# Kernel tuning notes

Measured on AMD Instinct MI355X. Metric: run time of the kernel, lower is better.

## Reference

```python
import jax, jax.numpy as jnp
import numpy as np

N, E, G = 50000, 800000, 128      # nodes, edges, graphs
IN, H, OUT = 128, 128, 2          # feature dims
K, L = 3, 3                       # Chebyshev order, num conv layers
EPS = 1e-5


def setup_inputs() -> dict:
    key = jax.random.key(0)
    ks = jax.random.split(key, 10)
    x = jax.random.normal(ks[0], (N, IN), dtype=jnp.float32)
    edge_index = jax.random.randint(ks[1], (2, E), 0, N, dtype=jnp.int64)
    batch = jnp.sort(jax.random.randint(ks[2], (N,), 0, G, dtype=jnp.int64))
    w_in = jax.random.normal(ks[3], (IN, H), dtype=jnp.float32) * 0.05
    b_in = jnp.zeros((H,), jnp.float32)
    ln_g = jnp.ones((H,), jnp.float32)
    ln_b = jnp.zeros((H,), jnp.float32)
    cheb_w = jax.random.normal(ks[4], (L, K, H, H), dtype=jnp.float32) * 0.05
    cheb_b = jnp.zeros((L, H), jnp.float32)
    bn_g = jnp.ones((L, H), jnp.float32)
    bn_b = jnp.zeros((L, H), jnp.float32)
    w1 = jax.random.normal(ks[5], (H, H // 2), dtype=jnp.float32) * 0.05
    b1 = jnp.zeros((H // 2,), jnp.float32)
    w2 = jax.random.normal(ks[6], (H // 2, OUT), dtype=jnp.float32) * 0.05
    b2 = jnp.zeros((OUT,), jnp.float32)
    return dict(x=x, w_in=w_in, b_in=b_in, ln_g=ln_g, ln_b=ln_b,
                cheb_w=cheb_w, cheb_b=cheb_b, bn_g=bn_g, bn_b=bn_b,
                w1=w1, b1=b1, w2=w2, b2=b2,
                edge_index=edge_index, batch=batch)


def reference(x, w_in, b_in, ln_g, ln_b, cheb_w, cheb_b, bn_g, bn_b,
              w1, b1, w2, b2, edge_index, batch):
    src, dst = edge_index[0], edge_index[1]

    # ChebConv scaled Laplacian with lambda_max=2, sym norm:
    # L_hat = -D^{-1/2} A D^{-1/2}  (self-loop terms cancel in PyG's __norm__)
    deg = jax.ops.segment_sum(jnp.ones((E,), x.dtype), src, num_segments=N)
    dinv = jnp.where(deg > 0, jax.lax.rsqrt(jnp.maximum(deg, 1.0)), 0.0)
    w_edge = -dinv[src] * dinv[dst]  # [E]

    def spmm(h):  # y_i = sum_{(j->i)} w_edge * h_j
        return jax.ops.segment_sum(w_edge[:, None] * h[src], dst, num_segments=N)

    # node_embed: Linear -> LayerNorm -> ReLU (dropout p used in eval => identity)
    h = x @ w_in + b_in
    mu = h.mean(-1, keepdims=True)
    var = h.var(-1, keepdims=True)
    h = (h - mu) * jax.lax.rsqrt(var + EPS) * ln_g + ln_b
    h = jax.nn.relu(h)

    hiddens = [h]
    for l in range(L):
        # Chebyshev recurrence: T0 = h, T1 = L_hat h, Tk = 2 L_hat T_{k-1} - T_{k-2}
        tx0 = h
        out = tx0 @ cheb_w[l, 0]
        tx1 = spmm(tx0)
        out = out + tx1 @ cheb_w[l, 1]
        for k in range(2, K):
            tx2 = 2.0 * spmm(tx1) - tx0
            out = out + tx2 @ cheb_w[l, k]
            tx0, tx1 = tx1, tx2
        out = out + cheb_b[l]
        # BatchNorm1d over nodes (training-mode batch statistics, biased var)
        m = out.mean(0)
        v = out.var(0)
        out = (out - m) * jax.lax.rsqrt(v + EPS) * bn_g[l] + bn_b[l]
        h = jax.nn.relu(out)
        hiddens.append(h)

    # Laplacian (Dirichlet) regularization over all hidden states
    reg = jnp.float32(0.0)
    for hh in hiddens:
        diff = hh[src] - hh[dst]              # [E, H]
        reg = reg + jnp.mean(jnp.sum(diff * diff, axis=-1))
    reg = reg / len(hiddens)

    # global mean pool over batch assignment
    counts = jax.ops.segment_sum(jnp.ones((N,), x.dtype), batch, num_segments=G)
    gsum = jax.ops.segment_sum(h, batch, num_segments=G)
    gmean = gsum / jnp.maximum(counts, 1.0)[:, None]

    z = jax.nn.relu(gmean @ w1 + b1)
    logits = z @ w2 + b2
    return logits, reg
```

## Files before the change

### kernel.cpp

```cpp
#include <hip/hip_runtime.h>
#include <hip/hip_bf16.h>

#define NNODES 50000
#define NEDGES 800000
#define NGRAPH 128
#define CAP 64
#define EPSV 1e-5f

typedef __attribute__((ext_vector_type(8))) short bf16x8;
typedef __attribute__((ext_vector_type(8))) unsigned short us16x8;
typedef __attribute__((ext_vector_type(4))) float f32x4;
typedef __attribute__((ext_vector_type(2))) float f32x2;

__device__ __forceinline__ unsigned short f2bf(float f) {
    unsigned u = __float_as_uint(f);
    return (unsigned short)((u + 0x7fffu + ((u >> 16) & 1u)) >> 16);
}
__device__ __forceinline__ float bf2f(unsigned short h) {
    return __uint_as_float(((unsigned)h) << 16);
}
__device__ __forceinline__ unsigned pk4_fp8(float a, float b, float c, float d) {
    int w = __builtin_amdgcn_cvt_pk_fp8_f32(a, b, 0, false);
    w = __builtin_amdgcn_cvt_pk_fp8_f32(c, d, w, true);
    return (unsigned)w;
}

__global__ void fillA_kernel(const int* __restrict__ src, const int* __restrict__ dst,
                             int* __restrict__ outdeg, int* __restrict__ indeg,
                             unsigned* __restrict__ slot, int E) {
    int e = blockIdx.x * blockDim.x + threadIdx.x;
    if (e < E) {
        int s = src[e];
        int d = dst[e];
        atomicAdd(&outdeg[s], 1);
        int pos = atomicAdd(&indeg[d], 1);
        if (pos < CAP) slot[(size_t)d * CAP + pos] = (unsigned)s;
    }
}

__global__ void dinv_gstart_kernel(const int* __restrict__ outdeg, float* __restrict__ dinv,
                                   const int* __restrict__ batch, int* __restrict__ gstart, int n) {
    int i = blockIdx.x * blockDim.x + threadIdx.x;
    if (i < n) {
        int d = outdeg[i];
        dinv[i] = (d > 0) ? rsqrtf((float)d) : 0.0f;
    }
    if (blockIdx.x == 0 && threadIdx.x <= NGRAPH) {
        int g = threadIdx.x;
        int lo = 0, hi = n;
        while (lo < hi) {
            int mid = (lo + hi) >> 1;
            if (batch[mid] < g) lo = mid + 1; else hi = mid;
        }
        gstart[g] = lo;
    }
}

__global__ void pack_kernel(unsigned* __restrict__ slot, const int* __restrict__ indeg,
                            const float* __restrict__ dinv, int total) {
    int i = blockIdx.x * blockDim.x + threadIdx.x;
    if (i >= total) return;
    int node = i >> 6, k = i & (CAP - 1);
    int cnt = min(indeg[node], CAP);
    if (k < cnt) {
        unsigned idx = slot[i];
        slot[i] = idx | ((unsigned)f2bf(dinv[idx]) << 16);
    }
}

__global__ void wprep_kernel(const float* __restrict__ w_in, const float* __restrict__ cheb_w,
                             unsigned short* __restrict__ Wsp) {
    int p = blockIdx.x;
    int t = threadIdx.x;
    for (int s8 = 0; s8 < 8; ++s8) {
        int slot = s8 * 256 + t;
        int kc = slot >> 9, ct = (slot >> 6) & 7, lane = slot & 63;
        int q = lane >> 4, nn = lane & 15;
        unsigned short* o = Wsp + ((size_t)p * 2048 + slot) * 16;
#pragma unroll
        for (int j = 0; j < 8; ++j) {
            int k = kc * 32 + q * 8 + j, c = ct * 16 + nn;
            float v;
            if (p == 0) {
                v = w_in[k * 128 + c];
            } else {
                int pl = (p - 1) / 3, kk = (p - 1) % 3;
                v = cheb_w[((size_t)(pl * 3 + kk) * 128 + k) * 128 + c];
                if (kk == 0) v -= cheb_w[((size_t)(pl * 3 + 2) * 128 + k) * 128 + c];
                else if (kk == 2) v *= 2.f;
            }
            unsigned short hi = f2bf(v);
            o[j] = hi;
            o[8 + j] = f2bf(v - bf2f(hi));
        }
    }
}

template <int NPARTS, int EPI, int AF32>
__global__ __launch_bounds__(256) void gemm_mfma(
    const void* __restrict__ A0v, const void* __restrict__ A1v, const void* __restrict__ A2v,
    const unsigned short* __restrict__ Wsp, const float* __restrict__ bias,
    unsigned short* __restrict__ out16,
    const float* __restrict__ g0, const float* __restrict__ b0,
    float* __restrict__ colsum, float* __restrict__ colsumsq, int n) {
    __shared__ float red[256];
    int t = threadIdx.x, w = t >> 6, l = t & 63;
    int m = l & 15, qk = l >> 4;
    int rowA = blockIdx.x * 64 + w * 16 + m;
    red[t] = 0.f;
    __syncthreads();

    f32x4 acc[8];
#pragma unroll
    for (int ct = 0; ct < 8; ++ct) acc[ct] = (f32x4){0.f, 0.f, 0.f, 0.f};

    bool valid = rowA < n;
#pragma unroll
    for (int p = 0; p < NPARTS; ++p) {
#pragma unroll
        for (int kc = 0; kc < 4; ++kc) {
            bf16x8 ah, al;
            if (AF32) {
                const float* arow = (const float*)A0v;
                if (p == 1) arow = (const float*)A1v;
                if (p == 2) arow = (const float*)A2v;
                arow += (size_t)rowA * 128;
                float4 x0, x1;
                if (valid) {
                    x0 = *(const float4*)&arow[kc * 32 + qk * 8];
                    x1 = *(const float4*)&arow[kc * 32 + qk * 8 + 4];
                } else {
                    x0 = make_float4(0.f, 0.f, 0.f, 0.f); x1 = x0;
                }
                float xs[8] = {x0.x, x0.y, x0.z, x0.w, x1.x, x1.y, x1.z, x1.w};
#pragma unroll
                for (int j = 0; j < 8; ++j) {
                    unsigned short hi = f2bf(xs[j]);
                    ah[j] = (short)hi;
                    al[j] = (short)f2bf(xs[j] - bf2f(hi));
                }
            } else {
                const unsigned short* arow = (const unsigned short*)A0v;
                if (p == 1) arow = (const unsigned short*)A1v;
                if (p == 2) arow = (const unsigned short*)A2v;
                arow += (size_t)rowA * 128;
                if (valid) ah = *(const bf16x8*)&arow[kc * 32 + qk * 8];
                else ah = (bf16x8){0, 0, 0, 0, 0, 0, 0, 0};
            }
            const unsigned short* wb = Wsp + ((size_t)((p * 4 + kc) * 8) * 64 + l) * 16;
#pragma unroll
            for (int ct = 0; ct < 8; ++ct) {
                bf16x8 bh = *(const bf16x8*)(wb + (size_t)ct * 64 * 16);
                bf16x8 bl = *(const bf16x8*)(wb + (size_t)ct * 64 * 16 + 8);
                acc[ct] = __builtin_amdgcn_mfma_f32_16x16x32_bf16(ah, bh, acc[ct], 0, 0, 0);
                if (AF32)
                    acc[ct] = __builtin_amdgcn_mfma_f32_16x16x32_bf16(al, bh, acc[ct], 0, 0, 0);
                acc[ct] = __builtin_amdgcn_mfma_f32_16x16x32_bf16(ah, bl, acc[ct], 0, 0, 0);
            }
        }
    }

    int rowC0 = blockIdx.x * 64 + w * 16 + qk * 4;
    if (EPI == 0) {
        float rs[4] = {0.f, 0.f, 0.f, 0.f}, rss[4] = {0.f, 0.f, 0.f, 0.f};
#pragma unroll
        for (int ct = 0; ct < 8; ++ct) {
            float b = bias[ct * 16 + m];
#pragma unroll
            for (int j = 0; j < 4; ++j) {
                float v = acc[ct][j] + b;
                acc[ct][j] = v;
                rs[j] += v; rss[j] += v * v;
            }
        }
#pragma unroll
        for (int off = 1; off < 16; off <<= 1) {
#pragma unroll
            for (int j = 0; j < 4; ++j) {
                rs[j] += __shfl_xor(rs[j], off, 64);
                rss[j] += __shfl_xor(rss[j], off, 64);
            }
        }
        float mean[4], rstd[4];
#pragma unroll
        for (int j = 0; j < 4; ++j) {
            mean[j] = rs[j] * (1.f / 128.f);
            float var = rss[j] * (1.f / 128.f) - mean[j] * mean[j];
            rstd[j] = rsqrtf(var + EPSV);
        }
#pragma unroll
        for (int ct = 0; ct < 8; ++ct) {
            int c = ct * 16 + m;
            float gg = g0[c], bb = b0[c];
#pragma unroll
            for (int j = 0; j < 4; ++j) {
                int gr = rowC0 + j;
                if (gr < n) {
                    float x = (acc[ct][j] - mean[j]) * rstd[j] * gg + bb;
                    x = fmaxf(x, 0.f);
                    out16[(size_t)gr * 128 + c] = f2bf(x);
                }
            }
        }
    } else {
#pragma unroll
        for (int ct = 0; ct < 8; ++ct) {
            int c = ct * 16 + m;
            float b = bias[c];
            float s = 0.f, ss = 0.f;
#pragma unroll
            for (int j = 0; j < 4; ++j) {
                int gr = rowC0 + j;
                if (gr < n) {
                    float v = acc[ct][j] + b;
                    out16[(size_t)gr * 128 + c] = f2bf(v);
                    s += v; ss += v * v;
                }
            }
            s += __shfl_xor(s, 16, 64);  ss += __shfl_xor(ss, 16, 64);
            s += __shfl_xor(s, 32, 64);  ss += __shfl_xor(ss, 32, 64);
            if (qk == 0) {
                atomicAdd(&red[c], s);
                atomicAdd(&red[128 + c], ss);
            }
        }
        __syncthreads();
        if (t < 128) {
            atomicAdd(&colsum[t], red[t]);
            atomicAdd(&colsumsq[t], red[128 + t]);
        }
    }
}

__global__ void repack8_kernel(const unsigned short* __restrict__ h16,
                               unsigned char* __restrict__ h8, int total8) {
    int i = blockIdx.x * blockDim.x + threadIdx.x;
    if (i >= total8) return;
    us16x8 a = ((const us16x8*)h16)[i];
    uint2 o;
    o.x = pk4_fp8(bf2f(a[0]), bf2f(a[1]), bf2f(a[2]), bf2f(a[3]));
    o.y = pk4_fp8(bf2f(a[4]), bf2f(a[5]), bf2f(a[6]), bf2f(a[7]));
    ((uint2*)h8)[i] = o;
}

template <int MODE>
__global__ void spmm_g(const unsigned char* __restrict__ g8,
                       const unsigned short* __restrict__ self16,
                       unsigned short* __restrict__ dst16, unsigned char* __restrict__ dst8,
                       const unsigned* __restrict__ slot,
                       const float* __restrict__ dinv,
                       const int* __restrict__ outdeg, const int* __restrict__ indeg,
                       int n, double* __restrict__ norm_slots, double* __restrict__ cross_slots) {
    int w = (int)((blockIdx.x * (unsigned)blockDim.x + threadIdx.x) >> 6);
    if (w >= n) return;
    int lane = threadIdx.x & 63;
    int g = lane >> 4;
    int q = lane & 15;
    int cnt = min(indeg[w], CAP);
    float hi[8];
    if (MODE != 1) {
        us16x8 a = *(const us16x8*)&self16[(size_t)w * 128 + q * 8];
#pragma unroll
        for (int j = 0; j < 8; ++j) hi[j] = bf2f(a[j]);
    }
    float acc[8];
#pragma unroll
    for (int j = 0; j < 8; ++j) acc[j] = 0.f;
    float cr = 0.f;
    unsigned cw = 0;
    if (lane < cnt) cw = slot[(size_t)w * CAP + lane];
    int idx = (int)(cw & 0xFFFFu);
    float dv = bf2f((unsigned short)(cw >> 16));
    int iters = (cnt + 31) >> 5;
    for (int it = 0; it < iters; ++it) {
        int sb = (it << 5) + (g << 3);
        int jj[8]; float dd[8];
#pragma unroll
        for (int u = 0; u < 8; ++u) {
            jj[u] = __shfl(idx, sb + u, 64);
            dd[u] = __shfl(dv, sb + u, 64);
        }
        uint2 uu[8];
#pragma unroll
        for (int u = 0; u < 8; ++u) {
            uu[u] = make_uint2(0, 0);
            if (sb + u < cnt) uu[u] = *(const uint2*)&g8[(size_t)jj[u] * 128 + q * 8];
        }
#pragma unroll
        for (int u = 0; u < 8; ++u) {
            f32x2 l0 = __builtin_amdgcn_cvt_pk_f32_fp8(uu[u].x, false);
            f32x2 h0 = __builtin_amdgcn_cvt_pk_f32_fp8(uu[u].x, true);
            f32x2 l1 = __builtin_amdgcn_cvt_pk_f32_fp8(uu[u].y, false);
            f32x2 h1 = __builtin_amdgcn_cvt_pk_f32_fp8(uu[u].y, true);
            float v[8] = {l0.x, l0.y, h0.x, h0.y, l1.x, l1.y, h1.x, h1.y};
            if (MODE != 2) {
#pragma unroll
                for (int j = 0; j < 8; ++j) acc[j] += dd[u] * v[j];
            }
            if (MODE != 1) {
#pragma unroll
                for (int j = 0; j < 8; ++j) cr += hi[j] * v[j];
            }
        }
    }
    if (MODE != 2) {
#pragma unroll
        for (int j = 0; j < 8; ++j) {
            acc[j] += __shfl_xor(acc[j], 16, 64);
            acc[j] += __shfl_xor(acc[j], 32, 64);
        }
        if (g == 0) {
            float di = dinv[w];
            float v[8];
            us16x8 o;
#pragma unroll
            for (int j = 0; j < 8; ++j) { v[j] = -di * acc[j]; o[j] = f2bf(v[j]); }
            *(us16x8*)&dst16[(size_t)w * 128 + q * 8] = o;
            if (MODE == 0) {
                uint2 o8;
                o8.x = pk4_fp8(v[0], v[1], v[2], v[3]);
                o8.y = pk4_fp8(v[4], v[5], v[6], v[7]);
                *(uint2*)&dst8[(size_t)w * 128 + q * 8] = o8;
            }
        }
    }
    if (MODE != 1) {
        float nt = 0.f;
#pragma unroll
        for (int j = 0; j < 8; ++j) nt += hi[j] * hi[j];
        nt *= 0.25f;
        for (int off = 32; off > 0; off >>= 1) {
            cr += __shfl_down(cr, off, 64);
            nt += __shfl_down(nt, off, 64);
        }
        if (lane == 0) {
            int slotid = w & 255;
            atomicAdd(&cross_slots[slotid], (double)cr);
            atomicAdd(&norm_slots[slotid], (double)nt * (double)(outdeg[w] + indeg[w]));
        }
    }
}

__global__ void bnrelu_kernel(const unsigned short* __restrict__ ob16,
                              const float* __restrict__ colsum, const float* __restrict__ colsumsq,
                              const float* __restrict__ bn_g, const float* __restrict__ bn_b,
                              unsigned short* __restrict__ h16, unsigned char* __restrict__ h8,
                              int n, int total4) {
    __shared__ float ssc[128], ssh[128];
    int t = threadIdx.x;
    if (t < 128) {
        float m = colsum[t] / (float)n;
        float v = colsumsq[t] / (float)n - m * m;
        float sc = bn_g[t] * rsqrtf(v + EPSV);
        ssc[t] = sc;
        ssh[t] = bn_b[t] - m * sc;
    }
    __syncthreads();
    int i = blockIdx.x * blockDim.x + t;
    if (i >= total4) return;
    ushort4 o = ((const ushort4*)ob16)[i];
    int c = (i * 4) & 127;
    float4 r;
    r.x = fmaxf(bf2f(o.x) * ssc[c + 0] + ssh[c + 0], 0.f);
    r.y = fmaxf(bf2f(o.y) * ssc[c + 1] + ssh[c + 1], 0.f);
    r.z = fmaxf(bf2f(o.z) * ssc[c + 2] + ssh[c + 2], 0.f);
    r.w = fmaxf(bf2f(o.w) * ssc[c + 3] + ssh[c + 3], 0.f);
    ushort4 u = make_ushort4(f2bf(r.x), f2bf(r.y), f2bf(r.z), f2bf(r.w));
    ((ushort4*)h16)[i] = u;
    ((unsigned*)h8)[i] = pk4_fp8(r.x, r.y, r.z, r.w);
}

__global__ void poolmlp_kernel(const unsigned short* __restrict__ h16, const int* __restrict__ start,
                               const float* __restrict__ w1, const float* __restrict__ b1,
                               const float* __restrict__ w2, const float* __restrict__ b2,
                               const double* __restrict__ norm_slots,
                               const double* __restrict__ cross_slots,
                               float* __restrict__ out) {
    __shared__ float sm[2][128];
    __shared__ float gm[128];
    int g = blockIdx.x, t = threadIdx.x;
    int half = t >> 7, c = t & 127;
    int s = start[g], e = start[g + 1];
    float acc = 0.f;
    for (int r = s + half; r < e; r += 2) acc += bf2f(h16[(size_t)r * 128 + c]);
    sm[half][c] = acc;
    __syncthreads();
    if (t < 128) {
        float cnt = fmaxf((float)(e - s), 1.f);
        gm[t] = (sm[0][t] + sm[1][t]) / cnt;
    }
    __syncthreads();
    if (t < 64) {
        float z = b1[t];
        for (int k = 0; k < 128; ++k) z += gm[k] * w1[(size_t)k * 64 + t];
        z = fmaxf(z, 0.f);
        float p0 = z * w2[t * 2 + 0];
        float p1 = z * w2[t * 2 + 1];
        for (int off = 32; off > 0; off >>= 1) {
            p0 += __shfl_down(p0, off, 64);
            p1 += __shfl_down(p1, off, 64);
        }
        if (t == 0) {
            out[g * 2 + 0] = p0 + b2[0];
            out[g * 2 + 1] = p1 + b2[1];
        }
    } else if (g == 0 && t < 128) {
        int l = t - 64;
        double ns = 0.0, cs = 0.0;
        for (int i = l; i < 256; i += 64) { ns += norm_slots[i]; cs += cross_slots[i]; }
        for (int off = 32; off > 0; off >>= 1) {
            ns += __shfl_down(ns, off, 64);
            cs += __shfl_down(cs, off, 64);
        }
        if (l == 0) out[256] = (float)((ns - 2.0 * cs) / ((double)NEDGES * 4.0));
    }
}

extern "C" void kernel_launch(void* const* d_in, const int* in_sizes, int n_in,
                              void* d_out, int out_size, void* d_ws, size_t ws_size,
                              hipStream_t stream) {
    const float* x      = (const float*)d_in[0];
    const float* w_in   = (const float*)d_in[1];
    const float* b_in   = (const float*)d_in[2];
    const float* ln_g   = (const float*)d_in[3];
    const float* ln_b   = (const float*)d_in[4];
    const float* cheb_w = (const float*)d_in[5];
    const float* cheb_b = (const float*)d_in[6];
    const float* bn_g   = (const float*)d_in[7];
    const float* bn_b   = (const float*)d_in[8];
    const float* w1     = (const float*)d_in[9];
    const float* b1     = (const float*)d_in[10];
    const float* w2     = (const float*)d_in[11];
    const float* b2     = (const float*)d_in[12];
    const int*   eidx   = (const int*)d_in[13];
    const int*   batch  = (const int*)d_in[14];
    const int* src = eidx;
    const int* dst = eidx + NEDGES;
    float* out = (float*)d_out;

    char* ws = (char*)d_ws;
    size_t off = 0;
    auto alloc = [&](size_t bytes) -> void* {
        void* p = ws + off;
        off = (off + bytes + 255) & ~(size_t)255;
        return p;
    };
    unsigned short* ob16 = (unsigned short*)alloc((size_t)NNODES * 128 * 2);
    unsigned short* h16  = (unsigned short*)alloc((size_t)NNODES * 128 * 2);
    unsigned short* t116 = (unsigned short*)alloc((size_t)NNODES * 128 * 2);
    unsigned short* s16  = (unsigned short*)alloc((size_t)NNODES * 128 * 2);
    unsigned char*  h8   = (unsigned char*)alloc((size_t)NNODES * 128);
    unsigned char*  t18  = (unsigned char*)alloc((size_t)NNODES * 128);
    unsigned short* Wsp  = (unsigned short*)alloc((size_t)10 * 2048 * 16 * 2);
    int* degs     = (int*)alloc((size_t)2 * NNODES * 4);
    int* outdeg   = degs;
    int* indeg    = degs + NNODES;
    float* dinv   = (float*)alloc((size_t)NNODES * 4);
    unsigned* slot = (unsigned*)alloc((size_t)NNODES * CAP * 4);
    int* gstart   = (int*)alloc((size_t)(NGRAPH + 1) * 4);
    float* colstats = (float*)alloc(768 * 4 + 512 * 8);
    double* dslots  = (double*)(colstats + 768);
    double* norm_slots  = dslots;
    double* cross_slots = dslots + 256;

    hipMemsetAsync(degs, 0, (size_t)2 * NNODES * 4, stream);
    hipMemsetAsync(colstats, 0, 768 * 4 + 512 * 8, stream);

    int tE = (NEDGES + 255) / 256;
    int tN = (NNODES + 255) / 256;
    fillA_kernel<<<tE, 256, 0, stream>>>(src, dst, outdeg, indeg, slot, NEDGES);
    dinv_gstart_kernel<<<tN, 256, 0, stream>>>(outdeg, dinv, batch, gstart, NNODES);
    pack_kernel<<<(NNODES * CAP + 255) / 256, 256, 0, stream>>>(slot, indeg, dinv, NNODES * CAP);
    wprep_kernel<<<10, 256, 0, stream>>>(w_in, cheb_w, Wsp);

    int gemmBlocks = (NNODES + 63) / 64;
    int waveBlocks = (NNODES * 64 + 255) / 256;
    int total4 = NNODES * 128 / 4;
    int total8 = NNODES * 128 / 8;

    gemm_mfma<1, 0, 1><<<gemmBlocks, 256, 0, stream>>>(x, nullptr, nullptr, Wsp, b_in, h16,
                                                       ln_g, ln_b, nullptr, nullptr, NNODES);
    repack8_kernel<<<(total8 + 255) / 256, 256, 0, stream>>>(h16, h8, total8);

    for (int l = 0; l < 3; ++l) {
        float* colsum = colstats + 256 * l;
        float* colsumsq = colsum + 128;
        spmm_g<0><<<waveBlocks, 256, 0, stream>>>(h8, h16, t116, t18, slot, dinv,
                                                  outdeg, indeg, NNODES, norm_slots, cross_slots);
        spmm_g<1><<<waveBlocks, 256, 0, stream>>>(t18, nullptr, s16, nullptr, slot, dinv,
                                                  outdeg, indeg, NNODES, nullptr, nullptr);
        gemm_mfma<3, 1, 0><<<gemmBlocks, 256, 0, stream>>>(h16, t116, s16,
            Wsp + (size_t)(1 + 3 * l) * 2048 * 16, cheb_b + (size_t)l * 128, ob16,
            nullptr, nullptr, colsum, colsumsq, NNODES);
        bnrelu_kernel<<<(total4 + 255) / 256, 256, 0, stream>>>(ob16, colsum, colsumsq,
            bn_g + (size_t)l * 128, bn_b + (size_t)l * 128, h16, h8, NNODES, total4);
    }
    spmm_g<2><<<waveBlocks, 256, 0, stream>>>(h8, h16, nullptr, nullptr, slot, dinv,
                                              outdeg, indeg, NNODES, norm_slots, cross_slots);

    poolmlp_kernel<<<NGRAPH, 256, 0, stream>>>(h16, gstart, w1, b1, w2, b2,
                                               norm_slots, cross_slots, out);
}
```

Before: 738.5 us.

## Map four nodes per wavefront in SpMM with 16-lane groups per node

The SpMM/Dirichlet kernel now gives each node a 16-lane group, so one wavefront handles four nodes instead of one. Each group loads its own edge slots in chunks of 16 and gathers neighbour rows itself. This removes the cross-group xor-shuffle reduction, the duplicated self-row reads and the 0.25 norm correction. It targets the lanes that sat idle when a node's in-degree (about 16 on average) was far below the 32-edge iteration width. The cost is more divergence between groups with different degrees, and each group now walks its edges serially in chunks of 16.

```diff
diff --git a/kernel.cpp b/kernel.cpp
--- a/kernel.cpp
+++ b/kernel.cpp
@@ -251,43 +251,45 @@
                        const float* __restrict__ dinv,
                        const int* __restrict__ outdeg, const int* __restrict__ indeg,
                        int n, double* __restrict__ norm_slots, double* __restrict__ cross_slots) {
-    int w = (int)((blockIdx.x * (unsigned)blockDim.x + threadIdx.x) >> 6);
-    if (w >= n) return;
     int lane = threadIdx.x & 63;
     int g = lane >> 4;
     int q = lane & 15;
-    int cnt = min(indeg[w], CAP);
+    int w = (int)((blockIdx.x * (unsigned)blockDim.x + threadIdx.x) >> 6) * 4 + g;
+    bool active = w < n;
+    int cnt = active ? min(indeg[w], CAP) : 0;
+    size_t rbase = (size_t)w * 128 + q * 8;
     float hi[8];
     if (MODE != 1) {
-        us16x8 a = *(const us16x8*)&self16[(size_t)w * 128 + q * 8];
-#pragma unroll
-        for (int j = 0; j < 8; ++j) hi[j] = bf2f(a[j]);
+#pragma unroll
+        for (int j = 0; j < 8; ++j) hi[j] = 0.f;
+        if (active) {
+            us16x8 a = *(const us16x8*)&self16[rbase];
+#pragma unroll
+            for (int j = 0; j < 8; ++j) hi[j] = bf2f(a[j]);
+        }
     }
     float acc[8];
 #pragma unroll
     for (int j = 0; j < 8; ++j) acc[j] = 0.f;
     float cr = 0.f;
-    unsigned cw = 0;
-    if (lane < cnt) cw = slot[(size_t)w * CAP + lane];
-    int idx = (int)(cw & 0xFFFFu);
-    float dv = bf2f((unsigned short)(cw >> 16));
-    int iters = (cnt + 31) >> 5;
-    for (int it = 0; it < iters; ++it) {
-        int sb = (it << 5) + (g << 3);
-        int jj[8]; float dd[8];
-#pragma unroll
-        for (int u = 0; u < 8; ++u) {
-            jj[u] = __shfl(idx, sb + u, 64);
-            dd[u] = __shfl(dv, sb + u, 64);
-        }
-        uint2 uu[8];
-#pragma unroll
-        for (int u = 0; u < 8; ++u) {
+    size_t sbase = (size_t)w * CAP;
+#pragma unroll
+    for (int c = 0; c < 4; ++c) {
+        if (c * 16 >= cnt) break;
+        unsigned cw = (c * 16 + q < cnt) ? slot[sbase + c * 16 + q] : 0u;
+        int mycnt = min(cnt - c * 16, 16);
+        uint2 uu[16];
+        float dd[16];
+#pragma unroll
+        for (int u = 0; u < 16; ++u) {
+            unsigned cwu = __shfl(cw, (g << 4) + u, 64);
+            int j = (int)(cwu & 0xFFFFu);
+            dd[u] = bf2f((unsigned short)(cwu >> 16));
             uu[u] = make_uint2(0, 0);
-            if (sb + u < cnt) uu[u] = *(const uint2*)&g8[(size_t)jj[u] * 128 + q * 8];
-        }
-#pragma unroll
-        for (int u = 0; u < 8; ++u) {
+            if (u < mycnt) uu[u] = *(const uint2*)&g8[(size_t)j * 128 + q * 8];
+        }
+#pragma unroll
+        for (int u = 0; u < 16; ++u) {
             f32x2 l0 = __builtin_amdgcn_cvt_pk_f32_fp8(uu[u].x, false);
             f32x2 h0 = __builtin_amdgcn_cvt_pk_f32_fp8(uu[u].x, true);
             f32x2 l1 = __builtin_amdgcn_cvt_pk_f32_fp8(uu[u].y, false);
@@ -303,37 +305,30 @@
             }
         }
     }
-    if (MODE != 2) {
-#pragma unroll
-        for (int j = 0; j < 8; ++j) {
-            acc[j] += __shfl_xor(acc[j], 16, 64);
-            acc[j] += __shfl_xor(acc[j], 32, 64);
-        }
-        if (g == 0) {
-            float di = dinv[w];
-            float v[8];
-            us16x8 o;
-#pragma unroll
-            for (int j = 0; j < 8; ++j) { v[j] = -di * acc[j]; o[j] = f2bf(v[j]); }
-            *(us16x8*)&dst16[(size_t)w * 128 + q * 8] = o;
-            if (MODE == 0) {
-                uint2 o8;
-                o8.x = pk4_fp8(v[0], v[1], v[2], v[3]);
-                o8.y = pk4_fp8(v[4], v[5], v[6], v[7]);
-                *(uint2*)&dst8[(size_t)w * 128 + q * 8] = o8;
-            }
+    if (MODE != 2 && active) {
+        float di = dinv[w];
+        float v[8];
+        us16x8 o;
+#pragma unroll
+        for (int j = 0; j < 8; ++j) { v[j] = -di * acc[j]; o[j] = f2bf(v[j]); }
+        *(us16x8*)&dst16[rbase] = o;
+        if (MODE == 0) {
+            uint2 o8;
+            o8.x = pk4_fp8(v[0], v[1], v[2], v[3]);
+            o8.y = pk4_fp8(v[4], v[5], v[6], v[7]);
+            *(uint2*)&dst8[(size_t)w * 128 + q * 8] = o8;
         }
     }
     if (MODE != 1) {
         float nt = 0.f;
 #pragma unroll
         for (int j = 0; j < 8; ++j) nt += hi[j] * hi[j];
-        nt *= 0.25f;
-        for (int off = 32; off > 0; off >>= 1) {
-            cr += __shfl_down(cr, off, 64);
-            nt += __shfl_down(nt, off, 64);
-        }
-        if (lane == 0) {
+#pragma unroll
+        for (int off = 8; off > 0; off >>= 1) {
+            cr += __shfl_down(cr, off, 16);
+            nt += __shfl_down(nt, off, 16);
+        }
+        if (q == 0 && active) {
             int slotid = w & 255;
             atomicAdd(&cross_slots[slotid], (double)cr);
             atomicAdd(&norm_slots[slotid], (double)nt * (double)(outdeg[w] + indeg[w]));
@@ -474,7 +469,8 @@
     wprep_kernel<<<10, 256, 0, stream>>>(w_in, cheb_w, Wsp);
 
     int gemmBlocks = (NNODES + 63) / 64;
-    int waveBlocks = (NNODES * 64 + 255) / 256;
+    int nodes4 = (NNODES + 3) / 4;
+    int spmmBlocks = (nodes4 * 64 + 255) / 256;
     int total4 = NNODES * 128 / 4;
     int total8 = NNODES * 128 / 8;
 
@@ -485,9 +481,9 @@
     for (int l = 0; l < 3; ++l) {
         float* colsum = colstats + 256 * l;
         float* colsumsq = colsum + 128;
-        spmm_g<0><<<waveBlocks, 256, 0, stream>>>(h8, h16, t116, t18, slot, dinv,
+        spmm_g<0><<<spmmBlocks, 256, 0, stream>>>(h8, h16, t116, t18, slot, dinv,
                                                   outdeg, indeg, NNODES, norm_slots, cross_slots);
-        spmm_g<1><<<waveBlocks, 256, 0, stream>>>(t18, nullptr, s16, nullptr, slot, dinv,
+        spmm_g<1><<<spmmBlocks, 256, 0, stream>>>(t18, nullptr, s16, nullptr, slot, dinv,
                                                   outdeg, indeg, NNODES, nullptr, nullptr);
         gemm_mfma<3, 1, 0><<<gemmBlocks, 256, 0, stream>>>(h16, t116, s16,
             Wsp + (size_t)(1 + 3 * l) * 2048 * 16, cheb_b + (size_t)l * 128, ob16,
@@ -495,7 +491,7 @@
         bnrelu_kernel<<<(total4 + 255) / 256, 256, 0, stream>>>(ob16, colsum, colsumsq,
             bn_g + (size_t)l * 128, bn_b + (size_t)l * 128, h16, h8, NNODES, total4);
     }
-    spmm_g<2><<<waveBlocks, 256, 0, stream>>>(h8, h16, nullptr, nullptr, slot, dinv,
+    spmm_g<2><<<spmmBlocks, 256, 0, stream>>>(h8, h16, nullptr, nullptr, slot, dinv,
                                               outdeg, indeg, NNODES, norm_slots, cross_slots);
 
     poolmlp_kernel<<<NGRAPH, 256, 0, stream>>>(h16, gstart, w1, b1, w2, b2,
```

After: 695.8 us. 1.06x faster.
